# Kernel tuning notes

Measured on AMD Instinct MI355X. Metric: run time of the kernel, lower is better.

## Reference

```python
import jax, jax.numpy as jnp
import numpy as np

N, D, H, L, B, DFF = 100000, 256, 8, 64, 4096, 1024
HD = D // H  # head_dim
EPS = 1e-5


def _xavier(k, shape):
    lim = (6.0 / (shape[0] + shape[1])) ** 0.5
    return jax.random.uniform(k, shape, jnp.float32, -lim, lim)


def setup_inputs() -> dict:
    key = jax.random.key(0)
    ks = jax.random.split(key, 12)
    batch = jax.random.randint(ks[0], (B,), 0, N)
    nei_idx = jax.random.randint(ks[1], (B, L), 0, N)
    # faithful to neis_ = [[k] + neighbor[k] ...]: self node is first neighbor
    nei_idx = nei_idx.at[:, 0].set(batch)
    lengths = jax.random.randint(ks[2], (B,), 1, L + 1)
    nei_mask = jnp.arange(L)[None, :] >= lengths[:, None]  # True = NaN padding
    embeddings = jax.random.normal(ks[3], (N, D), jnp.float32)
    return {
        "batch": batch, "nei_idx": nei_idx, "nei_mask": nei_mask,
        "embeddings": embeddings,
        "Wq": _xavier(ks[4], (D, D)), "bq": jnp.zeros((D,), jnp.float32),
        "Wk": _xavier(ks[5], (D, D)), "bk": jnp.zeros((D,), jnp.float32),
        "Wv": _xavier(ks[6], (D, D)), "bv": jnp.zeros((D,), jnp.float32),
        "Wo": _xavier(ks[7], (D, D)), "bo": jnp.zeros((D,), jnp.float32),
        "W1": _xavier(ks[8], (D, DFF)), "b1": jnp.zeros((DFF,), jnp.float32),
        "W2": _xavier(ks[9], (DFF, D)), "b2": jnp.zeros((D,), jnp.float32),
        "ln1_w": jnp.ones((D,), jnp.float32), "ln1_b": jnp.zeros((D,), jnp.float32),
        "ln2_w": jnp.ones((D,), jnp.float32), "ln2_b": jnp.zeros((D,), jnp.float32),
    }


def _layer_norm(y, w, b):
    mu = y.mean(-1, keepdims=True)
    var = ((y - mu) ** 2).mean(-1, keepdims=True)
    return (y - mu) / jnp.sqrt(var + EPS) * w + b


def reference(batch, nei_idx, nei_mask, embeddings,
              Wq, bq, Wk, bk, Wv, bv, Wo, bo,
              W1, b1, W2, b2, ln1_w, ln1_b, ln2_w, ln2_b):
    x = embeddings[batch]        # [B, D]  query-node embeddings
    nei = embeddings[nei_idx]    # [B, L, D] gathered (padded) neighbor embeds
    q = ((x @ Wq + bq) * (HD ** -0.5)).reshape(B, H, HD)
    k = (nei @ Wk + bk).reshape(B, L, H, HD)
    v = (nei @ Wv + bv).reshape(B, L, H, HD)
    scores = jnp.einsum('bhd,blhd->bhl', q, k)          # single-query attn
    scores = jnp.where(nei_mask[:, None, :], -jnp.inf, scores)
    att = jax.nn.softmax(scores, axis=-1)               # [B, H, L]
    attout = jnp.einsum('bhl,blhd->bhd', att, v).reshape(B, D) @ Wo + bo
    s = _layer_norm(x + attout, ln1_w, ln1_b)
    # note: original applies relu after BOTH linear1 and linear2
    f = jax.nn.relu(jax.nn.relu(s @ W1 + b1) @ W2 + b2)
    return _layer_norm(s + f, ln2_w, ln2_b)
```

## Files before the change

### kernel.cpp

```cpp
#include <hip/hip_runtime.h>
#include <hip/hip_bf16.h>
#include <math.h>

#define BQ   4096
#define D    256
#define NH   8
#define HD   32
#define LN_  64
#define DFF  1024
#define EPSV 1e-5f
#define QSCALE 0.17677669529663687f

typedef __attribute__((ext_vector_type(8))) short short8;
typedef __attribute__((ext_vector_type(4))) float f32x4;

#define ESWZ(row, byte) ((byte) ^ (((row) & 7) << 4))

__device__ __forceinline__ float wave_sum(float v){
#pragma unroll
  for (int off = 32; off; off >>= 1) v += __shfl_xor(v, off, 64);
  return v;
}
__device__ __forceinline__ unsigned short f2bf(float f){
  unsigned int u = __float_as_uint(f);
  unsigned int r = (u + 0x7FFFu + ((u >> 16) & 1u)) >> 16;
  return (unsigned short)r;
}

__global__ __launch_bounds__(256) void k_prep(
    const float* __restrict__ Wq, const float* __restrict__ Wk,
    const float* __restrict__ Wv, const float* __restrict__ Wo,
    const float* __restrict__ W1, const float* __restrict__ W2,
    const float* __restrict__ bq, const float* __restrict__ bv,
    const float* __restrict__ bo,
    const int* __restrict__ batch, const float* __restrict__ emb,
    const unsigned int* __restrict__ maskw,
    unsigned short* __restrict__ W1t, unsigned short* __restrict__ W2t,
    unsigned short* __restrict__ Mt, unsigned short* __restrict__ Gt,
    float* __restrict__ pb, float* __restrict__ bo2,
    float* __restrict__ X, unsigned short* __restrict__ Xb,
    int* __restrict__ flagsArr){
  __shared__ float smem[4224];
  const int bid = blockIdx.x;
  const int tid = threadIdx.x;

  if (bid < 128){
    const float* src; unsigned short* dst; int K, N, t0;
    if (bid < 64){ src = W1; dst = W1t; K = 256;  N = 1024; t0 = bid; }
    else         { src = W2; dst = W2t; K = 1024; N = 256;  t0 = bid - 64; }
    const int ntx = N / 64;
    const int k0 = (t0 / ntx) * 64, n0 = (t0 % ntx) * 64;
    float (*Ts)[65] = (float(*)[65])smem;
    {
      int r = tid >> 2, c4 = (tid & 3) * 16;
#pragma unroll
      for (int i = 0; i < 4; i++)
        *(float4*)&Ts[r][c4 + i * 4] = *(const float4*)(src + (size_t)(k0 + r) * N + n0 + c4 + i * 4);
    }
    __syncthreads();
    {
      int n = tid >> 2, kc = (tid & 3) * 16;
      unsigned int pk[8];
#pragma unroll
      for (int i = 0; i < 8; i++){
        unsigned int lo = f2bf(Ts[kc + 2 * i][n]);
        unsigned int hi = f2bf(Ts[kc + 2 * i + 1][n]);
        pk[i] = lo | (hi << 16);
      }
      unsigned short* orow = dst + (size_t)(n0 + n) * K + k0 + kc;
      *(uint4*)(orow)     = *(uint4*)&pk[0];
      *(uint4*)(orow + 8) = *(uint4*)&pk[4];
    }
    return;
  }
  if (bid < 256){
    int t0 = bid - 128;
    int hd0 = (t0 & 31) * 64, c0 = (t0 >> 5) * 64;
    int h = hd0 >> 8, d0 = hd0 & 255;
    float (*WqS)[33] = (float(*)[33])smem;
    float (*WkS)[33] = (float(*)[33])(smem + 64 * 33);
#pragma unroll
    for (int s = 0; s < 2; s++){
      int idx = tid + s * 256;
      int row = idx >> 3, c4 = (idx & 7) * 4;
      *(float4*)&WqS[row][c4] = *(const float4*)(Wq + (size_t)(c0 + row) * 256 + h * 32 + c4);
      *(float4*)&WkS[row][c4] = *(const float4*)(Wk + (size_t)(d0 + row) * 256 + h * 32 + c4);
    }
    __syncthreads();
    int jo = (tid >> 4) * 4, io = (tid & 15) * 4;
    float acc[4][4];
#pragma unroll
    for (int j = 0; j < 4; j++)
#pragma unroll
      for (int i = 0; i < 4; i++) acc[j][i] = 0.f;
#pragma unroll
    for (int t = 0; t < 32; t++){
#pragma unroll
      for (int j = 0; j < 4; j++){
        float kv = WkS[jo + j][t];
#pragma unroll
        for (int i = 0; i < 4; i++) acc[j][i] = fmaf(kv, WqS[io + i][t], acc[j][i]);
      }
    }
#pragma unroll
    for (int j = 0; j < 4; j++){
      uint2 o;
      o.x = (unsigned)f2bf(acc[j][0] * QSCALE) | ((unsigned)f2bf(acc[j][1] * QSCALE) << 16);
      o.y = (unsigned)f2bf(acc[j][2] * QSCALE) | ((unsigned)f2bf(acc[j][3] * QSCALE) << 16);
      *(uint2*)(Mt + (size_t)(hd0 + jo + j) * 256 + c0 + io) = o;
    }
    if (c0 == 0 && tid < 64){
      float s = 0.f;
#pragma unroll
      for (int t = 0; t < 32; t++) s = fmaf(WkS[tid][t], bq[h * 32 + t], s);
      pb[hd0 + tid] = s * QSCALE;
    }
    return;
  }
  if (bid < 384){
    int t0 = bid - 256;
    int hd0 = (t0 & 31) * 64, n0 = (t0 >> 5) * 64;
    int h = hd0 >> 8, d0 = hd0 & 255;
    float (*WvS)[33] = (float(*)[33])smem;
    float (*WoS)[65] = (float(*)[65])(smem + 64 * 33);
#pragma unroll
    for (int s = 0; s < 2; s++){
      int idx = tid + s * 256;
      int row = idx >> 3, c4 = (idx & 7) * 4;
      *(float4*)&WvS[row][c4] = *(const float4*)(Wv + (size_t)(d0 + row) * 256 + h * 32 + c4);
      int row2 = idx >> 4, c42 = (idx & 15) * 4;
      *(float4*)&WoS[row2][c42] = *(const float4*)(Wo + (size_t)(h * 32 + row2) * 256 + n0 + c42);
    }
    __syncthreads();
    int jo = (tid >> 4) * 4, io = (tid & 15) * 4;
    float acc[4][4];
#pragma unroll
    for (int i = 0; i < 4; i++)
#pragma unroll
      for (int j = 0; j < 4; j++) acc[i][j] = 0.f;
#pragma unroll
    for (int t = 0; t < 32; t++){
#pragma unroll
      for (int i = 0; i < 4; i++){
        float ov = WoS[t][io + i];
#pragma unroll
        for (int j = 0; j < 4; j++) acc[i][j] = fmaf(ov, WvS[jo + j][t], acc[i][j]);
      }
    }
#pragma unroll
    for (int i = 0; i < 4; i++){
      uint2 o;
      o.x = (unsigned)f2bf(acc[i][0]) | ((unsigned)f2bf(acc[i][1]) << 16);
      o.y = (unsigned)f2bf(acc[i][2]) | ((unsigned)f2bf(acc[i][3]) << 16);
      *(uint2*)(Gt + (size_t)(n0 + io + i) * 2048 + hd0 + jo) = o;
    }
    return;
  }
  if (bid == 384){
    int n = tid;
    float s = bo[n];
    for (int j = 0; j < 256; j++) s = fmaf(bv[j], Wo[(size_t)j * 256 + n], s);
    bo2[n] = s;
    return;
  }
  if (bid < 641){
    int* df = (int*)smem;
    if (tid == 0) df[0] = 0;
    __syncthreads();
    int idx = (bid - 385) * 256 + tid;
    unsigned int v = maskw[idx];
    int bits = 0;
    if (v == 0x3F800000u) bits = 2;
    else if (v & 0xFFFFFF00u) bits = 1;
    int b2 = __any(bits & 2) ? 2 : 0;
    int b1 = __any(bits & 1) ? 1 : 0;
    if ((tid & 63) == 0 && (b1 | b2)) atomicOr(df, b1 | b2);
    __syncthreads();
    if (tid == 0) flagsArr[bid - 385] = df[0];
    return;
  }
  {
    int gid = (bid - 641) * 256 + tid;
    int b = gid >> 6, c = gid & 63;
    float4 v = ((const float4*)(emb + (size_t)batch[b] * D))[c];
    ((float4*)(X + (size_t)b * D))[c] = v;
    uint2 p;
    p.x = (unsigned)f2bf(v.x) | ((unsigned)f2bf(v.y) << 16);
    p.y = (unsigned)f2bf(v.z) | ((unsigned)f2bf(v.w) << 16);
    ((uint2*)Xb)[gid] = p;
  }
}

template<int BM, int BN, int EPI, bool OUTBF>
__global__ __launch_bounds__(256) void k_mgemm(const unsigned short* __restrict__ A,
                                               const unsigned short* __restrict__ Bt,
                                               const float* __restrict__ bias,
                                               void* __restrict__ Cout,
                                               int M, int N, int K){
  constexpr int BK = 64;
  constexpr int WM = BM / 2, WN = BN / 2;
  constexpr int MR = WM / 16, NR = WN / 16;
  constexpr int AIT = BM * 8 / 256;
  constexpr int BIT = BN * 8 / 256;
  __shared__ __align__(16) unsigned short As[BM * BK];
  __shared__ __align__(16) unsigned short Bs[BN * BK];
  char* ab = (char*)As; char* bb = (char*)Bs;
  const int tid = threadIdx.x;
  const int w = tid >> 6, lane = tid & 63;
  const int wm = w >> 1, wn = w & 1;
  const int gx = gridDim.x;
  const int nwg = gx * gridDim.y;
  const int o = blockIdx.y * gx + blockIdx.x;
  const int lin = (o & 7) * (nwg >> 3) + (o >> 3);
  const int row0 = (lin / gx) * BM, col0 = (lin % gx) * BN;
  f32x4 acc[MR][NR];
#pragma unroll
  for (int m = 0; m < MR; m++)
#pragma unroll
    for (int n = 0; n < NR; n++) acc[m][n] = (f32x4){0.f, 0.f, 0.f, 0.f};

  for (int k0 = 0; k0 < K; k0 += BK){
#pragma unroll
    for (int s = 0; s < AIT; s++){
      int c = s * 256 + tid;
      int r = c >> 3, jj = c & 7;
      uint4 v = *(const uint4*)(A + (size_t)(row0 + r) * K + k0 + jj * 8);
      *(uint4*)(ab + ESWZ(r, r * 128 + jj * 16)) = v;
    }
#pragma unroll
    for (int s = 0; s < BIT; s++){
      int c = s * 256 + tid;
      int r = c >> 3, jj = c & 7;
      uint4 v = *(const uint4*)(Bt + (size_t)(col0 + r) * K + k0 + jj * 8);
      *(uint4*)(bb + ESWZ(r, r * 128 + jj * 16)) = v;
    }
    __syncthreads();
#pragma unroll
    for (int kk = 0; kk < 2; kk++){
      short8 af[MR], bf[NR];
#pragma unroll
      for (int m = 0; m < MR; m++){
        int r = wm * WM + m * 16 + (lane & 15);
        af[m] = *(const short8*)(ab + ESWZ(r, r * 128 + (kk * 4 + (lane >> 4)) * 16));
      }
#pragma unroll
      for (int n = 0; n < NR; n++){
        int r = wn * WN + n * 16 + (lane & 15);
        bf[n] = *(const short8*)(bb + ESWZ(r, r * 128 + (kk * 4 + (lane >> 4)) * 16));
      }
#pragma unroll
      for (int m = 0; m < MR; m++)
#pragma unroll
        for (int n = 0; n < NR; n++)
          acc[m][n] = __builtin_amdgcn_mfma_f32_16x16x32_bf16(af[m], bf[n], acc[m][n], 0, 0, 0);
    }
    __syncthreads();
  }
#pragma unroll
  for (int m = 0; m < MR; m++){
#pragma unroll
    for (int n = 0; n < NR; n++){
      int col = col0 + wn * WN + n * 16 + (lane & 15);
      float bsv = bias[col];
      int rbase = row0 + wm * WM + m * 16 + (lane >> 4) * 4;
#pragma unroll
      for (int r = 0; r < 4; r++){
        float v = acc[m][n][r] + bsv;
        if (EPI == 3) v = fmaxf(v, 0.f);
        if (OUTBF) ((unsigned short*)Cout)[(size_t)(rbase + r) * N + col] = f2bf(v);
        else       ((float*)Cout)[(size_t)(rbase + r) * N + col] = v;
      }
    }
  }
}

__global__ __launch_bounds__(256) void k_attn(const int* __restrict__ nei_idx,
                                              const void* __restrict__ nei_mask,
                                              const int* __restrict__ flagsArr,
                                              const float* __restrict__ emb,
                                              const unsigned short* __restrict__ Pb,
                                              unsigned short* __restrict__ Cb){
  const int b = blockIdx.x;
  const int tid = threadIdx.x;
  const int w = tid >> 6, lane = tid & 63;
  __shared__ __align__(16) unsigned short Ebf[64 * 256];
  __shared__ __align__(16) unsigned short Pl[9 * 256];
  __shared__ float sc[NH * LN_];
  __shared__ float mskv[LN_];
  __shared__ int   fred[4];
  char* eb = (char*)Ebf;
  char* pl = (char*)Pl;

  {
    int f = flagsArr[tid];
#pragma unroll
    for (int off = 32; off; off >>= 1) f |= __shfl_xor(f, off, 64);
    if (lane == 0) fred[w] = f;
  }
  float4 vr[16];
#pragma unroll
  for (int i = 0; i < 16; i++){
    int nid = nei_idx[(size_t)b * LN_ + w * 16 + i];
    vr[i] = ((const float4*)(emb + (size_t)nid * D))[lane];
  }
  {
    int r = tid >> 5, cb16 = (tid & 31) * 16;
    uint4 v = *(const uint4*)((const char*)Pb + (size_t)b * 4096 + r * 512 + cb16);
    *(uint4*)(pl + ESWZ(r, r * 512 + cb16)) = v;
  }
  if (tid < 64) *(uint2*)(pl + 8 * 512 + tid * 8) = make_uint2(0u, 0u);
  __syncthreads();

#pragma unroll
  for (int i = 0; i < 16; i++){
    int l = w * 16 + i;
    uint2 p;
    p.x = (unsigned)f2bf(vr[i].x) | ((unsigned)f2bf(vr[i].y) << 16);
    p.y = (unsigned)f2bf(vr[i].z) | ((unsigned)f2bf(vr[i].w) << 16);
    *(uint2*)(eb + ESWZ(l, l * 512 + lane * 8)) = p;
  }
  if (tid < LN_){
    int fl = fred[0] | fred[1] | fred[2] | fred[3];
    int mf = (fl & 2) ? 2 : ((fl & 1) ? 1 : 0);
    bool m;
    if (mf == 1)      m = ((const unsigned char*)nei_mask)[(size_t)b * LN_ + tid] != 0;
    else if (mf == 2) m = ((const float*)nei_mask)[(size_t)b * LN_ + tid] != 0.f;
    else              m = ((const int*)nei_mask)[(size_t)b * LN_ + tid] != 0;
    mskv[tid] = m ? 1.f : 0.f;
  }
  __syncthreads();

  {
    const int hr = lane & 15;
    const int arow = hr < 8 ? hr : 8;
    const int bl = w * 16 + (lane & 15);
    const int koff = (lane >> 4) * 16;
    f32x4 acc = {0.f, 0.f, 0.f, 0.f};
#pragma unroll
    for (int kk = 0; kk < 8; kk++){
      short8 af = *(const short8*)(pl + ESWZ(arow, arow * 512 + kk * 64 + koff));
      short8 bf = *(const short8*)(eb + ESWZ(bl, bl * 512 + kk * 64 + koff));
      acc = __builtin_amdgcn_mfma_f32_16x16x32_bf16(af, bf, acc, 0, 0, 0);
    }
    int hb = (lane >> 4) * 4;
    if (hb < 8){
#pragma unroll
      for (int r = 0; r < 4; r++) sc[(hb + r) * LN_ + bl] = acc[r];
    }
  }
  __syncthreads();

  {
    int h = tid >> 5, j = tid & 31;
    float v0 = mskv[j]      > 0.5f ? -INFINITY : sc[h * LN_ + j];
    float v1 = mskv[j + 32] > 0.5f ? -INFINITY : sc[h * LN_ + j + 32];
    float m = fmaxf(v0, v1);
#pragma unroll
    for (int off = 16; off; off >>= 1) m = fmaxf(m, __shfl_xor(m, off, 64));
    float e0 = __expf(v0 - m), e1 = __expf(v1 - m);
    float s = e0 + e1;
#pragma unroll
    for (int off = 16; off; off >>= 1) s += __shfl_xor(s, off, 64);
    float inv = 1.f / s;
    sc[h * LN_ + j]      = e0 * inv;
    sc[h * LN_ + j + 32] = e1 * inv;
  }
  __syncthreads();

  {
    const int h0 = w * 2, h1 = w * 2 + 1;
    float4 a0 = make_float4(0.f, 0.f, 0.f, 0.f);
    float4 a1 = make_float4(0.f, 0.f, 0.f, 0.f);
#pragma unroll 8
    for (int l = 0; l < 64; l++){
      uint2 raw = *(const uint2*)(eb + ESWZ(l, l * 512 + lane * 8));
      float e0 = __uint_as_float(raw.x << 16);
      float e1 = __uint_as_float(raw.x & 0xFFFF0000u);
      float e2 = __uint_as_float(raw.y << 16);
      float e3 = __uint_as_float(raw.y & 0xFFFF0000u);
      float t0 = sc[h0 * LN_ + l], t1 = sc[h1 * LN_ + l];
      a0.x = fmaf(t0, e0, a0.x); a0.y = fmaf(t0, e1, a0.y);
      a0.z = fmaf(t0, e2, a0.z); a0.w = fmaf(t0, e3, a0.w);
      a1.x = fmaf(t1, e0, a1.x); a1.y = fmaf(t1, e1, a1.y);
      a1.z = fmaf(t1, e2, a1.z); a1.w = fmaf(t1, e3, a1.w);
    }
    uint2 o0, o1;
    o0.x = (unsigned)f2bf(a0.x) | ((unsigned)f2bf(a0.y) << 16);
    o0.y = (unsigned)f2bf(a0.z) | ((unsigned)f2bf(a0.w) << 16);
    o1.x = (unsigned)f2bf(a1.x) | ((unsigned)f2bf(a1.y) << 16);
    o1.y = (unsigned)f2bf(a1.z) | ((unsigned)f2bf(a1.w) << 16);
    *(uint2*)((char*)Cb + (size_t)b * 4096 + h0 * 512 + lane * 8) = o0;
    *(uint2*)((char*)Cb + (size_t)b * 4096 + h1 * 512 + lane * 8) = o1;
  }
}

__global__ __launch_bounds__(256) void k_ln(const float* __restrict__ A,
                                            const float* __restrict__ Bv,
                                            const float* __restrict__ w,
                                            const float* __restrict__ bi,
                                            float* __restrict__ out,
                                            unsigned short* __restrict__ outb){
  const int row = blockIdx.x, tid = threadIdx.x;
  const int wv = tid >> 6, lane = tid & 63;
  __shared__ float red[8];
  float v = A[(size_t)row * D + tid] + Bv[(size_t)row * D + tid];
  float s = wave_sum(v);
  if (lane == 0) red[wv] = s;
  __syncthreads();
  float mu = (red[0] + red[1] + red[2] + red[3]) * (1.f / D);
  float d = v - mu;
  float s2 = wave_sum(d * d);
  if (lane == 0) red[4 + wv] = s2;
  __syncthreads();
  float var = (red[4] + red[5] + red[6] + red[7]) * (1.f / D);
  float res = d * rsqrtf(var + EPSV) * w[tid] + bi[tid];
  out[(size_t)row * D + tid] = res;
  if (outb) outb[(size_t)row * D + tid] = f2bf(res);
}

extern "C" void kernel_launch(void* const* d_in, const int* in_sizes, int n_in,
                              void* d_out, int out_size, void* d_ws, size_t ws_size,
                              hipStream_t stream){
  (void)in_sizes; (void)n_in; (void)out_size; (void)ws_size;
  const int*   batch    = (const int*)d_in[0];
  const int*   nei_idx  = (const int*)d_in[1];
  const void*  nei_mask = d_in[2];
  const float* emb      = (const float*)d_in[3];
  const float* Wq = (const float*)d_in[4];  const float* bq = (const float*)d_in[5];
  const float* Wk = (const float*)d_in[6];
  const float* Wv = (const float*)d_in[8];  const float* bv = (const float*)d_in[9];
  const float* Wo = (const float*)d_in[10]; const float* bo = (const float*)d_in[11];
  const float* W1 = (const float*)d_in[12]; const float* b1 = (const float*)d_in[13];
  const float* W2 = (const float*)d_in[14]; const float* b2 = (const float*)d_in[15];
  const float* ln1w = (const float*)d_in[16]; const float* ln1b = (const float*)d_in[17];
  const float* ln2w = (const float*)d_in[18]; const float* ln2b = (const float*)d_in[19];

  float* ws = (float*)d_ws;
  float* X  = ws;
  float* Y  = ws + (size_t)1 * 1048576;
  float* S  = ws + (size_t)2 * 1048576;
  float* F  = ws + (size_t)3 * 1048576;
  unsigned short* Pbf = (unsigned short*)(ws + (size_t)4 * 1048576);
  unsigned short* Cb  = Pbf;
  unsigned short* Sb  = (unsigned short*)(ws + (size_t)8 * 1048576);
  unsigned short* HHb = (unsigned short*)(ws + (size_t)9 * 1048576);
  unsigned short* Xb  = (unsigned short*)(ws + (size_t)11 * 1048576);
  char* wb = (char*)(ws + (size_t)12 * 1048576);
  unsigned short* W1t = (unsigned short*)(wb);
  unsigned short* W2t = (unsigned short*)(wb + (512u << 10));
  unsigned short* Mt  = (unsigned short*)(wb + (1024u << 10));
  unsigned short* Gt  = (unsigned short*)(wb + (2048u << 10));
  float* pbv  = (float*)(wb + (3072u << 10));
  float* bo2  = (float*)(wb + (3072u << 10) + 8192);
  int*   flagsArr = (int*)(wb + (3072u << 10) + 16384);
  float* out = (float*)d_out;

  k_prep<<<1665, 256, 0, stream>>>(Wq, Wk, Wv, Wo, W1, W2, bq, bv, bo,
                                   batch, emb, (const unsigned int*)nei_mask,
                                   W1t, W2t, Mt, Gt, pbv, bo2, X, Xb, flagsArr);
  k_mgemm<128, 64, 2, true><<<dim3(2048 / 64, BQ / 128), 256, 0, stream>>>(Xb, Mt, pbv, Pbf, BQ, 2048, 256);
  k_attn<<<BQ, 256, 0, stream>>>(nei_idx, nei_mask, flagsArr, emb, Pbf, Cb);
  k_mgemm<32, 64, 2, false><<<dim3(D / 64, BQ / 32), 256, 0, stream>>>(Cb, Gt, bo2, Y, BQ, D, 2048);
  k_ln<<<BQ, 256, 0, stream>>>(X, Y, ln1w, ln1b, S, Sb);
  k_mgemm<128, 64, 3, true><<<dim3(DFF / 64, BQ / 128), 256, 0, stream>>>(Sb, W1t, b1, HHb, BQ, DFF, 256);
  k_mgemm<32, 64, 3, false><<<dim3(D / 64, BQ / 32), 256, 0, stream>>>(HHb, W2t, b2, F, BQ, D, DFF);
  k_ln<<<BQ, 256, 0, stream>>>(S, F, ln2w, ln2b, out, nullptr);
}
```

Baseline: 122.3 us.

## Compute attention-weighted sum from fp32 registers with cross-wave LDS reduction

The weighted sum over neighbours now runs on each wave's 16 rows, which are still held in fp32 registers. Each wave accumulates all 8 heads for its rows, and the four per-wave partial results are summed through LDS, which reuses the bf16 embedding buffer. This removes the 64-row LDS re-read and bf16 unpacking of the old per-head loop, but adds a barrier, an LDS round trip, and 32 accumulator registers. It also switches bf16 packing to the library paired-conversion intrinsic and raises wave priority around the MFMA loop.

```diff
diff --git a/kernel.cpp b/kernel.cpp
--- a/kernel.cpp
+++ b/kernel.cpp
@@ -22,9 +22,12 @@
   return v;
 }
 __device__ __forceinline__ unsigned short f2bf(float f){
-  unsigned int u = __float_as_uint(f);
-  unsigned int r = (u + 0x7FFFu + ((u >> 16) & 1u)) >> 16;
-  return (unsigned short)r;
+  __hip_bfloat16 h = __float2bfloat16(f);
+  unsigned short r; __builtin_memcpy(&r, &h, 2); return r;
+}
+__device__ __forceinline__ unsigned pk2(float a, float b){
+  __hip_bfloat162 h = __float22bfloat162_rn(make_float2(a, b));
+  unsigned r; __builtin_memcpy(&r, &h, 4); return r;
 }
 
 __global__ __launch_bounds__(256) void k_prep(
@@ -62,11 +65,8 @@
       int n = tid >> 2, kc = (tid & 3) * 16;
       unsigned int pk[8];
 #pragma unroll
-      for (int i = 0; i < 8; i++){
-        unsigned int lo = f2bf(Ts[kc + 2 * i][n]);
-        unsigned int hi = f2bf(Ts[kc + 2 * i + 1][n]);
-        pk[i] = lo | (hi << 16);
-      }
+      for (int i = 0; i < 8; i++)
+        pk[i] = pk2(Ts[kc + 2 * i][n], Ts[kc + 2 * i + 1][n]);
       unsigned short* orow = dst + (size_t)(n0 + n) * K + k0 + kc;
       *(uint4*)(orow)     = *(uint4*)&pk[0];
       *(uint4*)(orow + 8) = *(uint4*)&pk[4];
@@ -105,8 +105,8 @@
 #pragma unroll
     for (int j = 0; j < 4; j++){
       uint2 o;
-      o.x = (unsigned)f2bf(acc[j][0] * QSCALE) | ((unsigned)f2bf(acc[j][1] * QSCALE) << 16);
-      o.y = (unsigned)f2bf(acc[j][2] * QSCALE) | ((unsigned)f2bf(acc[j][3] * QSCALE) << 16);
+      o.x = pk2(acc[j][0] * QSCALE, acc[j][1] * QSCALE);
+      o.y = pk2(acc[j][2] * QSCALE, acc[j][3] * QSCALE);
       *(uint2*)(Mt + (size_t)(hd0 + jo + j) * 256 + c0 + io) = o;
     }
     if (c0 == 0 && tid < 64){
@@ -150,8 +150,8 @@
 #pragma unroll
     for (int i = 0; i < 4; i++){
       uint2 o;
-      o.x = (unsigned)f2bf(acc[i][0]) | ((unsigned)f2bf(acc[i][1]) << 16);
-      o.y = (unsigned)f2bf(acc[i][2]) | ((unsigned)f2bf(acc[i][3]) << 16);
+      o.x = pk2(acc[i][0], acc[i][1]);
+      o.y = pk2(acc[i][2], acc[i][3]);
       *(uint2*)(Gt + (size_t)(n0 + io + i) * 2048 + hd0 + jo) = o;
     }
     return;
@@ -185,8 +185,8 @@
     float4 v = ((const float4*)(emb + (size_t)batch[b] * D))[c];
     ((float4*)(X + (size_t)b * D))[c] = v;
     uint2 p;
-    p.x = (unsigned)f2bf(v.x) | ((unsigned)f2bf(v.y) << 16);
-    p.y = (unsigned)f2bf(v.z) | ((unsigned)f2bf(v.w) << 16);
+    p.x = pk2(v.x, v.y);
+    p.y = pk2(v.z, v.w);
     ((uint2*)Xb)[gid] = p;
   }
 }
@@ -290,6 +290,7 @@
   __shared__ int   fred[4];
   char* eb = (char*)Ebf;
   char* pl = (char*)Pl;
+  float* pf = (float*)Ebf;
 
   {
     int f = flagsArr[tid];
@@ -315,8 +316,8 @@
   for (int i = 0; i < 16; i++){
     int l = w * 16 + i;
     uint2 p;
-    p.x = (unsigned)f2bf(vr[i].x) | ((unsigned)f2bf(vr[i].y) << 16);
-    p.y = (unsigned)f2bf(vr[i].z) | ((unsigned)f2bf(vr[i].w) << 16);
+    p.x = pk2(vr[i].x, vr[i].y);
+    p.y = pk2(vr[i].z, vr[i].w);
     *(uint2*)(eb + ESWZ(l, l * 512 + lane * 8)) = p;
   }
   if (tid < LN_){
@@ -336,12 +337,14 @@
     const int bl = w * 16 + (lane & 15);
     const int koff = (lane >> 4) * 16;
     f32x4 acc = {0.f, 0.f, 0.f, 0.f};
+    __builtin_amdgcn_s_setprio(1);
 #pragma unroll
     for (int kk = 0; kk < 8; kk++){
       short8 af = *(const short8*)(pl + ESWZ(arow, arow * 512 + kk * 64 + koff));
       short8 bf = *(const short8*)(eb + ESWZ(bl, bl * 512 + kk * 64 + koff));
       acc = __builtin_amdgcn_mfma_f32_16x16x32_bf16(af, bf, acc, 0, 0, 0);
     }
+    __builtin_amdgcn_s_setprio(0);
     int hb = (lane >> 4) * 4;
     if (hb < 8){
 #pragma unroll
@@ -368,29 +371,43 @@
   __syncthreads();
 
   {
-    const int h0 = w * 2, h1 = w * 2 + 1;
-    float4 a0 = make_float4(0.f, 0.f, 0.f, 0.f);
-    float4 a1 = make_float4(0.f, 0.f, 0.f, 0.f);
-#pragma unroll 8
-    for (int l = 0; l < 64; l++){
-      uint2 raw = *(const uint2*)(eb + ESWZ(l, l * 512 + lane * 8));
-      float e0 = __uint_as_float(raw.x << 16);
-      float e1 = __uint_as_float(raw.x & 0xFFFF0000u);
-      float e2 = __uint_as_float(raw.y << 16);
-      float e3 = __uint_as_float(raw.y & 0xFFFF0000u);
-      float t0 = sc[h0 * LN_ + l], t1 = sc[h1 * LN_ + l];
-      a0.x = fmaf(t0, e0, a0.x); a0.y = fmaf(t0, e1, a0.y);
-      a0.z = fmaf(t0, e2, a0.z); a0.w = fmaf(t0, e3, a0.w);
-      a1.x = fmaf(t1, e0, a1.x); a1.y = fmaf(t1, e1, a1.y);
-      a1.z = fmaf(t1, e2, a1.z); a1.w = fmaf(t1, e3, a1.w);
-    }
-    uint2 o0, o1;
-    o0.x = (unsigned)f2bf(a0.x) | ((unsigned)f2bf(a0.y) << 16);
-    o0.y = (unsigned)f2bf(a0.z) | ((unsigned)f2bf(a0.w) << 16);
-    o1.x = (unsigned)f2bf(a1.x) | ((unsigned)f2bf(a1.y) << 16);
-    o1.y = (unsigned)f2bf(a1.z) | ((unsigned)f2bf(a1.w) << 16);
-    *(uint2*)((char*)Cb + (size_t)b * 4096 + h0 * 512 + lane * 8) = o0;
-    *(uint2*)((char*)Cb + (size_t)b * 4096 + h1 * 512 + lane * 8) = o1;
+    float4 acc[NH];
+#pragma unroll
+    for (int h = 0; h < NH; h++) acc[h] = make_float4(0.f, 0.f, 0.f, 0.f);
+#pragma unroll
+    for (int i = 0; i < 16; i++){
+      int l = w * 16 + i;
+#pragma unroll
+      for (int h = 0; h < NH; h++){
+        float t = sc[h * LN_ + l];
+        acc[h].x = fmaf(t, vr[i].x, acc[h].x);
+        acc[h].y = fmaf(t, vr[i].y, acc[h].y);
+        acc[h].z = fmaf(t, vr[i].z, acc[h].z);
+        acc[h].w = fmaf(t, vr[i].w, acc[h].w);
+      }
+    }
+#pragma unroll
+    for (int h = 0; h < NH; h++)
+      *(float4*)&pf[w * 2048 + h * 256 + lane * 4] = acc[h];
+  }
+  __syncthreads();
+
+#pragma unroll
+  for (int s = 0; s < 2; s++){
+    int gi = tid + s * 256;
+    int h = gi >> 6, d4 = gi & 63;
+    float4 v0 = *(float4*)&pf[0 * 2048 + h * 256 + d4 * 4];
+    float4 v1 = *(float4*)&pf[1 * 2048 + h * 256 + d4 * 4];
+    float4 v2 = *(float4*)&pf[2 * 2048 + h * 256 + d4 * 4];
+    float4 v3 = *(float4*)&pf[3 * 2048 + h * 256 + d4 * 4];
+    float x = v0.x + v1.x + v2.x + v3.x;
+    float y = v0.y + v1.y + v2.y + v3.y;
+    float z = v0.z + v1.z + v2.z + v3.z;
+    float u = v0.w + v1.w + v2.w + v3.w;
+    uint2 o;
+    o.x = pk2(x, y);
+    o.y = pk2(z, u);
+    *(uint2*)(Cb + (size_t)b * 2048 + h * 256 + d4 * 4) = o;
   }
 }
 
```

After: 119.6 us. 2.2% less time.
